# Kernel tuning notes

Measured on AMD Instinct MI355X. Metric: run time of the kernel, lower is better.

## Reference

```python
import jax, jax.numpy as jnp
import numpy as np

N_NODES = 100000
N_EDGES = 3200000
F_IN = 512
HIDDEN = 16
N_LABELS = 64


def _degree_norms(edge_src, edge_dst, n):
    # DGL GraphConv norm='both': src side uses out-degree, dst side uses in-degree,
    # both clamped to min 1, raised to -1/2.
    ones = jnp.ones(edge_src.shape[0], dtype=jnp.float32)
    deg_out = jax.ops.segment_sum(ones, edge_src, num_segments=n)
    deg_in = jax.ops.segment_sum(ones, edge_dst, num_segments=n)
    norm_src = jax.lax.rsqrt(jnp.maximum(deg_out, 1.0))
    norm_dst = jax.lax.rsqrt(jnp.maximum(deg_in, 1.0))
    return norm_src, norm_dst


def setup_inputs() -> dict:
    key = jax.random.key(0)
    k_x, k_s, k_d, k_w1, k_b1, k_w2, k_b2 = jax.random.split(key, 7)
    features = jax.random.normal(k_x, (N_NODES, F_IN), dtype=jnp.float32)
    edge_src = jax.random.randint(k_s, (N_EDGES,), 0, N_NODES, dtype=jnp.int64)
    edge_dst = jax.random.randint(k_d, (N_EDGES,), 0, N_NODES, dtype=jnp.int64)
    # GraphConv params (glorot-ish scale)
    W1 = jax.random.normal(k_w1, (F_IN, HIDDEN), dtype=jnp.float32) * (1.0 / np.sqrt(F_IN))
    b1 = jnp.zeros((HIDDEN,), dtype=jnp.float32)
    W2 = jax.random.normal(k_w2, (HIDDEN, N_LABELS), dtype=jnp.float32) * (1.0 / np.sqrt(HIDDEN))
    b2 = jnp.zeros((N_LABELS,), dtype=jnp.float32)
    return {"features": features, "W1": W1, "b1": b1, "W2": W2, "b2": b2,
            "edge_src": edge_src, "edge_dst": edge_dst}


def reference(features, W1, b1, W2, b2, edge_src, edge_dst):
    n = features.shape[0]
    norm_src, norm_dst = _degree_norms(edge_src, edge_dst, n)

    # Layer 1: in_feats (512) > out_feats (16) -> DGL projects first, then aggregates.
    h = features * norm_src[:, None]          # [N, 512]
    h = h @ W1                                 # [N, 16]
    h = jax.ops.segment_sum(h[edge_src], edge_dst, num_segments=n)  # SpMM gather+scatter
    h = h * norm_dst[:, None] + b1
    h = jax.nn.relu(h)  # GraphConv activation; outer F.relu is idempotent

    # Layer 2: in_feats (16) <= out_feats (64) -> DGL aggregates first, then projects.
    h2 = h * norm_src[:, None]                 # [N, 16]
    h2 = jax.ops.segment_sum(h2[edge_src], edge_dst, num_segments=n)
    h2 = h2 * norm_dst[:, None]
    out = h2 @ W2 + b2                          # [N, 64]
    return out
```

## Files before the change

kernel.cpp:

```cpp
#include <hip/hip_runtime.h>

#define N_NODES 100000
#define N_EDGES 3200000
#define F_IN 512
#define HIDDEN 16
#define N_LABELS 64

#define BW 128
#define NBUCK ((N_NODES + BW - 1) / BW)
#define NCB 256
#define SCAN_N (NBUCK * NCB)
#define SCAN_BLKS ((SCAN_N + 1023) / 1024)
#define CAP 10240

__global__ __launch_bounds__(256) void count_kernel(
        const int* __restrict__ es, const int* __restrict__ ed,
        int* __restrict__ Msrc, int* __restrict__ Mdst) {
    __shared__ int h1[NBUCK], h2[NBUCK];
    const int tid = threadIdx.x, g = blockIdx.x;
    for (int i = tid; i < NBUCK; i += 256) { h1[i] = 0; h2[i] = 0; }
    __syncthreads();
    for (int i = g * 256 + tid; i < N_EDGES; i += NCB * 256) {
        atomicAdd(&h1[es[i] >> 7], 1);
        atomicAdd(&h2[ed[i] >> 7], 1);
    }
    __syncthreads();
    for (int i = tid; i < NBUCK; i += 256) {
        Msrc[i * NCB + g] = h1[i];
        Mdst[i * NCB + g] = h2[i];
    }
}

__global__ __launch_bounds__(256) void scanA_kernel(int* __restrict__ a, int* __restrict__ bsum) {
    __shared__ int s[256];
    const int tid = threadIdx.x;
    const int base = blockIdx.x * 1024 + tid * 4;
    int4 v = make_int4(0, 0, 0, 0);
    if (base + 3 < SCAN_N) v = *(const int4*)(a + base);
    else {
        if (base + 0 < SCAN_N) v.x = a[base + 0];
        if (base + 1 < SCAN_N) v.y = a[base + 1];
        if (base + 2 < SCAN_N) v.z = a[base + 2];
        if (base + 3 < SCAN_N) v.w = a[base + 3];
    }
    const int lsum = v.x + v.y + v.z + v.w;
    s[tid] = lsum;
    __syncthreads();
    for (int off = 1; off < 256; off <<= 1) {
        int t = (tid >= off) ? s[tid - off] : 0;
        __syncthreads();
        s[tid] += t;
        __syncthreads();
    }
    int e0 = s[tid] - lsum;
    int e1 = e0 + v.x, e2 = e1 + v.y, e3 = e2 + v.z;
    if (base + 3 < SCAN_N) *(int4*)(a + base) = make_int4(e0, e1, e2, e3);
    else {
        if (base + 0 < SCAN_N) a[base + 0] = e0;
        if (base + 1 < SCAN_N) a[base + 1] = e1;
        if (base + 2 < SCAN_N) a[base + 2] = e2;
        if (base + 3 < SCAN_N) a[base + 3] = e3;
    }
    if (tid == 255) bsum[blockIdx.x] = s[255];
}

__global__ void scanB_kernel(int* __restrict__ bsum) {
    __shared__ int s[256];
    const int tid = threadIdx.x;
    int v = (tid < SCAN_BLKS) ? bsum[tid] : 0;
    s[tid] = v;
    __syncthreads();
    for (int off = 1; off < 256; off <<= 1) {
        int t = (tid >= off) ? s[tid - off] : 0;
        __syncthreads();
        s[tid] += t;
        __syncthreads();
    }
    if (tid < SCAN_BLKS) bsum[tid] = s[tid] - v;
}

__global__ __launch_bounds__(256) void scanC_kernel(int* __restrict__ a, const int* __restrict__ bsum) {
    const int base = blockIdx.x * 1024 + threadIdx.x * 4;
    const int b = bsum[blockIdx.x];
    if (base + 3 < SCAN_N) {
        int4 v = *(int4*)(a + base);
        v.x += b; v.y += b; v.z += b; v.w += b;
        *(int4*)(a + base) = v;
    } else {
        for (int j = 0; j < 4; ++j) if (base + j < SCAN_N) a[base + j] += b;
    }
}

__global__ __launch_bounds__(256) void scatter_kernel(
        const int* __restrict__ es, const int* __restrict__ ed,
        const int* __restrict__ Ssrc, const int* __restrict__ Sdst,
        unsigned* __restrict__ pairs, unsigned char* __restrict__ srcb) {
    __shared__ int c1[NBUCK], c2[NBUCK];
    const int tid = threadIdx.x, g = blockIdx.x;
    for (int i = tid; i < NBUCK; i += 256) {
        c1[i] = Ssrc[i * NCB + g];
        c2[i] = Sdst[i * NCB + g];
    }
    __syncthreads();
    for (int i = g * 256 + tid; i < N_EDGES; i += NCB * 256) {
        int s = es[i], d = ed[i];
        int p2 = atomicAdd(&c2[d >> 7], 1);
        pairs[p2] = ((unsigned)(d & 127) << 17) | (unsigned)s;
        int p1 = atomicAdd(&c1[s >> 7], 1);
        srcb[p1] = (unsigned char)(s & 127);
    }
}

__global__ __launch_bounds__(256) void csr_kernel(
        const int* __restrict__ Sdst, unsigned* __restrict__ pairs,
        int* __restrict__ row_ptr, float* __restrict__ norm_dst) {
    __shared__ unsigned buf[CAP];
    __shared__ int hist[BW], scn[BW], cur[BW];
    const int b = blockIdx.x, tid = threadIdx.x;
    const int base  = Sdst[b * NCB];
    const int nextb = (b == NBUCK - 1) ? N_EDGES : Sdst[(b + 1) * NCB];
    const int nb = nextb - base;
    const bool fits = (nb <= CAP);
    if (tid < BW) hist[tid] = 0;
    __syncthreads();
    for (int i = tid; i < nb; i += 256) {
        unsigned pk = pairs[base + i];
        if (fits) buf[i] = pk;
        atomicAdd(&hist[pk >> 17], 1);
    }
    __syncthreads();
    if (tid < BW) scn[tid] = hist[tid];
    __syncthreads();
    for (int off = 1; off < BW; off <<= 1) {
        int t = 0;
        if (tid < BW && tid >= off) t = scn[tid - off];
        __syncthreads();
        if (tid < BW) scn[tid] += t;
        __syncthreads();
    }
    if (tid < BW) {
        int e = scn[tid] - hist[tid];
        cur[tid] = e;
        int node = b * BW + tid;
        if (node <= N_NODES) row_ptr[node] = base + e;
        if (node < N_NODES) norm_dst[node] = rsqrtf(fmaxf((float)hist[tid], 1.0f));
    }
    __syncthreads();
    if (fits) {
        for (int i = tid; i < nb; i += 256) {
            unsigned pk = buf[i];
            int pos = atomicAdd(&cur[pk >> 17], 1);
            pairs[base + pos] = pk & 0x1FFFFu;
        }
    } else {
        for (int i = tid; i < nb; i += 256)
            pairs[base + i] &= 0x1FFFFu;
    }
}

__global__ __launch_bounds__(256) void srcdeg_kernel(
        const int* __restrict__ Ssrc, const unsigned char* __restrict__ srcb,
        float* __restrict__ norm_src) {
    __shared__ int hist[BW];
    const int b = blockIdx.x, tid = threadIdx.x;
    const int base  = Ssrc[b * NCB];
    const int nextb = (b == NBUCK - 1) ? N_EDGES : Ssrc[(b + 1) * NCB];
    const int nb = nextb - base;
    if (tid < BW) hist[tid] = 0;
    __syncthreads();
    for (int i = tid; i < nb; i += 256)
        atomicAdd(&hist[srcb[base + i]], 1);
    __syncthreads();
    if (tid < BW) {
        int node = b * BW + tid;
        if (node < N_NODES) norm_src[node] = rsqrtf(fmaxf((float)hist[tid], 1.0f));
    }
}

#define P1_ROWS 256
#define P1_CH 32
#define KSPLIT 2
#define KH (F_IN / KSPLIT)
#define P1_CHUNKS (KH / P1_CH)
#define P1_BLKS ((N_NODES + P1_ROWS - 1) / P1_ROWS)

#define GLD16(gp, lp) __builtin_amdgcn_global_load_lds( \
    (const __attribute__((address_space(1))) unsigned int*)(gp), \
    (__attribute__((address_space(3))) unsigned int*)(lp), 16, 0, 0)

__global__ __launch_bounds__(256, 2) void proj1_kernel(
        const float* __restrict__ X, const float* __restrict__ W1,
        float* __restrict__ P0, float* __restrict__ P1) {
    __shared__ float xs[2][P1_ROWS * P1_CH];
    __shared__ float w1c[KH * HIDDEN];

    const int tid = threadIdx.x;
    const int node0 = blockIdx.x * P1_ROWS;
    const int z = blockIdx.y;

    const int srow0 = tid >> 3;
    const int scg   = tid & 7;
    const int wbase = tid & 192;

    for (int i = tid; i < KH * HIDDEN / 4; i += 256)
        ((float4*)w1c)[i] = ((const float4*)(W1 + (size_t)z * KH * HIDDEN))[i];

    {
        const float* Xc = X + (size_t)z * KH;
#pragma unroll
        for (int it = 0; it < 8; ++it) {
            int row = srow0 + it * 32;
            int grow = node0 + row;
            if (grow > N_NODES - 1) grow = N_NODES - 1;
            int cg = scg ^ ((row >> 2) & 7);
            const float* gp = Xc + (size_t)grow * F_IN + cg * 4;
            float* lp = &xs[0][(size_t)(it * 256 + wbase) * 4];
            GLD16(gp, lp);
        }
    }
    __syncthreads();

    const int rg = tid >> 2;
    const int kq = (tid & 3) * 4;

    float acc[4][4];
#pragma unroll
    for (int a = 0; a < 4; ++a)
#pragma unroll
        for (int b = 0; b < 4; ++b) acc[a][b] = 0.f;

    for (int cc = 0; cc < P1_CHUNKS; ++cc) {
        const int cur = cc & 1;

        if (cc + 1 < P1_CHUNKS) {
            const float* Xc = X + (size_t)z * KH + (size_t)(cc + 1) * P1_CH;
#pragma unroll
            for (int it = 0; it < 8; ++it) {
                int row = srow0 + it * 32;
                int grow = node0 + row;
                if (grow > N_NODES - 1) grow = N_NODES - 1;
                int cg = scg ^ ((row >> 2) & 7);
                const float* gp = Xc + (size_t)grow * F_IN + cg * 4;
                float* lp = &xs[cur ^ 1][(size_t)(it * 256 + wbase) * 4];
                GLD16(gp, lp);
            }
        }

        const float* xb = &xs[cur][0];
#pragma unroll
        for (int kk4 = 0; kk4 < 8; ++kk4) {
            float4 w0 = *((const float4*)&w1c[(cc * P1_CH + kk4 * 4 + 0) * HIDDEN + kq]);
            float4 w1 = *((const float4*)&w1c[(cc * P1_CH + kk4 * 4 + 1) * HIDDEN + kq]);
            float4 w2 = *((const float4*)&w1c[(cc * P1_CH + kk4 * 4 + 2) * HIDDEN + kq]);
            float4 w3 = *((const float4*)&w1c[(cc * P1_CH + kk4 * 4 + 3) * HIDDEN + kq]);
#pragma unroll
            for (int a = 0; a < 4; ++a) {
                int row = rg * 4 + a;
                int sw  = (row >> 2) & 7;
                float4 xv = *((const float4*)&xb[row * P1_CH + ((kk4 ^ sw) * 4)]);
                acc[a][0] += xv.x * w0.x; acc[a][1] += xv.x * w0.y;
                acc[a][2] += xv.x * w0.z; acc[a][3] += xv.x * w0.w;
                acc[a][0] += xv.y * w1.x; acc[a][1] += xv.y * w1.y;
                acc[a][2] += xv.y * w1.z; acc[a][3] += xv.y * w1.w;
                acc[a][0] += xv.z * w2.x; acc[a][1] += xv.z * w2.y;
                acc[a][2] += xv.z * w2.z; acc[a][3] += xv.z * w2.w;
                acc[a][0] += xv.w * w3.x; acc[a][1] += xv.w * w3.y;
                acc[a][2] += xv.w * w3.z; acc[a][3] += xv.w * w3.w;
            }
        }

        __syncthreads();
    }

    float* Pz = z ? P1 : P0;
#pragma unroll
    for (int a = 0; a < 4; ++a) {
        int gn = node0 + rg * 4 + a;
        if (gn < N_NODES)
            *((float4*)(Pz + (size_t)gn * HIDDEN + kq)) =
                make_float4(acc[a][0], acc[a][1], acc[a][2], acc[a][3]);
    }
}

__global__ void reduce1_kernel(const float* __restrict__ P0, const float* __restrict__ P1,
                               const float* __restrict__ norm_src, float* __restrict__ H1) {
    int gid = blockIdx.x * blockDim.x + threadIdx.x;
    if (gid < N_NODES * 4) {
        float4 a = ((const float4*)P0)[gid];
        float4 b = ((const float4*)P1)[gid];
        float ns = norm_src[gid >> 2];
        ((float4*)H1)[gid] = make_float4((a.x + b.x) * ns, (a.y + b.y) * ns,
                                         (a.z + b.z) * ns, (a.w + b.w) * ns);
    }
}

__global__ __launch_bounds__(256) void spmm1_kernel(
        const int* __restrict__ rp, const int* __restrict__ col,
        const float* __restrict__ H1, const float* __restrict__ norm_dst,
        const float* __restrict__ norm_src, const float* __restrict__ b1,
        float* __restrict__ H1b) {
    int tid = threadIdx.x;
    int node = blockIdx.x * 16 + (tid >> 4);
    int k = tid & 15;
    if (node >= N_NODES) return;
    int beg = rp[node], end = rp[node + 1];
    float acc = 0.f;
    int j = beg;
    for (; j + 3 < end; j += 4) {
        int s0 = col[j], s1 = col[j + 1], s2 = col[j + 2], s3 = col[j + 3];
        float v0 = H1[(size_t)s0 * HIDDEN + k];
        float v1 = H1[(size_t)s1 * HIDDEN + k];
        float v2 = H1[(size_t)s2 * HIDDEN + k];
        float v3 = H1[(size_t)s3 * HIDDEN + k];
        acc += v0 + v1 + v2 + v3;
    }
    for (; j < end; ++j) acc += H1[(size_t)col[j] * HIDDEN + k];
    float v = fmaxf(acc * norm_dst[node] + b1[k], 0.f) * norm_src[node];
    H1b[(size_t)node * HIDDEN + k] = v;
}

__global__ __launch_bounds__(256) void spmm2_final_kernel(
        const int* __restrict__ rp, const int* __restrict__ col,
        const float* __restrict__ H1b, const float* __restrict__ norm_dst,
        const float* __restrict__ W2, const float* __restrict__ b2,
        float* __restrict__ out) {
    __shared__ float w2s[HIDDEN * N_LABELS];
    int tid = threadIdx.x;
    ((float4*)w2s)[tid] = ((const float4*)W2)[tid];
    __syncthreads();

    int node = blockIdx.x * 16 + (tid >> 4);
    int k = tid & 15;
    if (node >= N_NODES) return;
    int beg = rp[node], end = rp[node + 1];
    float acc = 0.f;
    int j = beg;
    for (; j + 3 < end; j += 4) {
        int s0 = col[j], s1 = col[j + 1], s2 = col[j + 2], s3 = col[j + 3];
        float v0 = H1b[(size_t)s0 * HIDDEN + k];
        float v1 = H1b[(size_t)s1 * HIDDEN + k];
        float v2 = H1b[(size_t)s2 * HIDDEN + k];
        float v3 = H1b[(size_t)s3 * HIDDEN + k];
        acc += v0 + v1 + v2 + v3;
    }
    for (; j < end; ++j) acc += H1b[(size_t)col[j] * HIDDEN + k];
    acc *= norm_dst[node];

    float4 o = ((const float4*)b2)[k];
#pragma unroll
    for (int jj = 0; jj < HIDDEN; ++jj) {
        float hj = __shfl(acc, jj, 16);
        float4 w = *((const float4*)&w2s[jj * N_LABELS + 4 * k]);
        o.x += hj * w.x; o.y += hj * w.y; o.z += hj * w.z; o.w += hj * w.w;
    }
    ((float4*)out)[(size_t)node * 16 + k] = o;
}

extern "C" void kernel_launch(void* const* d_in, const int* in_sizes, int n_in,
                              void* d_out, int out_size, void* d_ws, size_t ws_size,
                              hipStream_t stream) {
    const float* X  = (const float*)d_in[0];
    const float* W1 = (const float*)d_in[1];
    const float* b1 = (const float*)d_in[2];
    const float* W2 = (const float*)d_in[3];
    const float* b2 = (const float*)d_in[4];
    const int* es   = (const int*)d_in[5];
    const int* ed   = (const int*)d_in[6];
    float* out = (float*)d_out;

    char* ws = (char*)d_ws;
    float* norm_src = (float*)ws;  ws += (size_t)N_NODES * 4;
    float* norm_dst = (float*)ws;  ws += (size_t)N_NODES * 4;
    int*   row_ptr  = (int*)ws;    ws += 400016;
    char*  R1 = ws;                ws += (size_t)N_NODES * HIDDEN * 4;
    char*  R2 = ws;                ws += (size_t)N_NODES * HIDDEN * 4;
    char*  R3 = ws;

    unsigned char* srcb = (unsigned char*)R1;
    float* P0  = (float*)R1;
    float* H1  = (float*)R1;
    int*   Sdst = (int*)R2;
    int*   Ssrc = (int*)(R2 + 800768);
    int*   bs1  = (int*)(R2 + 1601536);
    int*   bs2  = (int*)(R2 + 1602560);
    float* P1   = (float*)R2;
    float* H1b  = (float*)R2;
    unsigned* pairs = (unsigned*)R3;
    int*   col  = (int*)R3;

    count_kernel<<<NCB, 256, 0, stream>>>(es, ed, Ssrc, Sdst);
    scanA_kernel<<<SCAN_BLKS, 256, 0, stream>>>(Sdst, bs1);
    scanA_kernel<<<SCAN_BLKS, 256, 0, stream>>>(Ssrc, bs2);
    scanB_kernel<<<1, 256, 0, stream>>>(bs1);
    scanB_kernel<<<1, 256, 0, stream>>>(bs2);
    scanC_kernel<<<SCAN_BLKS, 256, 0, stream>>>(Sdst, bs1);
    scanC_kernel<<<SCAN_BLKS, 256, 0, stream>>>(Ssrc, bs2);
    scatter_kernel<<<NCB, 256, 0, stream>>>(es, ed, Ssrc, Sdst, pairs, srcb);
    csr_kernel<<<NBUCK, 256, 0, stream>>>(Sdst, pairs, row_ptr, norm_dst);
    srcdeg_kernel<<<NBUCK, 256, 0, stream>>>(Ssrc, srcb, norm_src);
    proj1_kernel<<<dim3(P1_BLKS, KSPLIT), 256, 0, stream>>>(X, W1, P0, P1);
    reduce1_kernel<<<(N_NODES * 4 + 255) / 256, 256, 0, stream>>>(P0, P1, norm_src, H1);
    spmm1_kernel<<<(N_NODES + 15) / 16, 256, 0, stream>>>(row_ptr, col, H1, norm_dst, norm_src, b1, H1b);
    spmm2_final_kernel<<<(N_NODES + 15) / 16, 256, 0, stream>>>(row_ptr, col, H1b, norm_dst, W2, b2, out);
}
```

Before: 598.8 us.

## Replace full CSR build with padded bucket scatter and shared-memory atomic aggregation

```diff
diff --git a/kernel.cpp b/kernel.cpp
--- a/kernel.cpp
+++ b/kernel.cpp
@@ -7,173 +7,36 @@
 #define N_LABELS 64
 
 #define BW 128
-#define NBUCK ((N_NODES + BW - 1) / BW)
+#define NBUCK 782
 #define NCB 256
-#define SCAN_N (NBUCK * NCB)
-#define SCAN_BLKS ((SCAN_N + 1023) / 1024)
-#define CAP 10240
-
-__global__ __launch_bounds__(256) void count_kernel(
+#define EPC (N_EDGES / NCB)
+#define PADB 4544
+
+__global__ __launch_bounds__(512) void scatter2_kernel(
         const int* __restrict__ es, const int* __restrict__ ed,
-        int* __restrict__ Msrc, int* __restrict__ Mdst) {
-    __shared__ int h1[NBUCK], h2[NBUCK];
+        int* __restrict__ gcur, int* __restrict__ deg,
+        unsigned* __restrict__ pairs) {
+    __shared__ int hist[NBUCK];
+    __shared__ int curL[NBUCK];
     const int tid = threadIdx.x, g = blockIdx.x;
-    for (int i = tid; i < NBUCK; i += 256) { h1[i] = 0; h2[i] = 0; }
-    __syncthreads();
-    for (int i = g * 256 + tid; i < N_EDGES; i += NCB * 256) {
-        atomicAdd(&h1[es[i] >> 7], 1);
-        atomicAdd(&h2[ed[i] >> 7], 1);
-    }
-    __syncthreads();
-    for (int i = tid; i < NBUCK; i += 256) {
-        Msrc[i * NCB + g] = h1[i];
-        Mdst[i * NCB + g] = h2[i];
-    }
-}
-
-__global__ __launch_bounds__(256) void scanA_kernel(int* __restrict__ a, int* __restrict__ bsum) {
-    __shared__ int s[256];
-    const int tid = threadIdx.x;
-    const int base = blockIdx.x * 1024 + tid * 4;
-    int4 v = make_int4(0, 0, 0, 0);
-    if (base + 3 < SCAN_N) v = *(const int4*)(a + base);
-    else {
-        if (base + 0 < SCAN_N) v.x = a[base + 0];
-        if (base + 1 < SCAN_N) v.y = a[base + 1];
-        if (base + 2 < SCAN_N) v.z = a[base + 2];
-        if (base + 3 < SCAN_N) v.w = a[base + 3];
-    }
-    const int lsum = v.x + v.y + v.z + v.w;
-    s[tid] = lsum;
-    __syncthreads();
-    for (int off = 1; off < 256; off <<= 1) {
-        int t = (tid >= off) ? s[tid - off] : 0;
-        __syncthreads();
-        s[tid] += t;
-        __syncthreads();
-    }
-    int e0 = s[tid] - lsum;
-    int e1 = e0 + v.x, e2 = e1 + v.y, e3 = e2 + v.z;
-    if (base + 3 < SCAN_N) *(int4*)(a + base) = make_int4(e0, e1, e2, e3);
-    else {
-        if (base + 0 < SCAN_N) a[base + 0] = e0;
-        if (base + 1 < SCAN_N) a[base + 1] = e1;
-        if (base + 2 < SCAN_N) a[base + 2] = e2;
-        if (base + 3 < SCAN_N) a[base + 3] = e3;
-    }
-    if (tid == 255) bsum[blockIdx.x] = s[255];
-}
-
-__global__ void scanB_kernel(int* __restrict__ bsum) {
-    __shared__ int s[256];
-    const int tid = threadIdx.x;
-    int v = (tid < SCAN_BLKS) ? bsum[tid] : 0;
-    s[tid] = v;
-    __syncthreads();
-    for (int off = 1; off < 256; off <<= 1) {
-        int t = (tid >= off) ? s[tid - off] : 0;
-        __syncthreads();
-        s[tid] += t;
-        __syncthreads();
-    }
-    if (tid < SCAN_BLKS) bsum[tid] = s[tid] - v;
-}
-
-__global__ __launch_bounds__(256) void scanC_kernel(int* __restrict__ a, const int* __restrict__ bsum) {
-    const int base = blockIdx.x * 1024 + threadIdx.x * 4;
-    const int b = bsum[blockIdx.x];
-    if (base + 3 < SCAN_N) {
-        int4 v = *(int4*)(a + base);
-        v.x += b; v.y += b; v.z += b; v.w += b;
-        *(int4*)(a + base) = v;
-    } else {
-        for (int j = 0; j < 4; ++j) if (base + j < SCAN_N) a[base + j] += b;
-    }
-}
-
-__global__ __launch_bounds__(256) void scatter_kernel(
-        const int* __restrict__ es, const int* __restrict__ ed,
-        const int* __restrict__ Ssrc, const int* __restrict__ Sdst,
-        unsigned* __restrict__ pairs, unsigned char* __restrict__ srcb) {
-    __shared__ int c1[NBUCK], c2[NBUCK];
-    const int tid = threadIdx.x, g = blockIdx.x;
-    for (int i = tid; i < NBUCK; i += 256) {
-        c1[i] = Ssrc[i * NCB + g];
-        c2[i] = Sdst[i * NCB + g];
-    }
-    __syncthreads();
-    for (int i = g * 256 + tid; i < N_EDGES; i += NCB * 256) {
-        int s = es[i], d = ed[i];
-        int p2 = atomicAdd(&c2[d >> 7], 1);
-        pairs[p2] = ((unsigned)(d & 127) << 17) | (unsigned)s;
-        int p1 = atomicAdd(&c1[s >> 7], 1);
-        srcb[p1] = (unsigned char)(s & 127);
-    }
-}
-
-__global__ __launch_bounds__(256) void csr_kernel(
-        const int* __restrict__ Sdst, unsigned* __restrict__ pairs,
-        int* __restrict__ row_ptr, float* __restrict__ norm_dst) {
-    __shared__ unsigned buf[CAP];
-    __shared__ int hist[BW], scn[BW], cur[BW];
-    const int b = blockIdx.x, tid = threadIdx.x;
-    const int base  = Sdst[b * NCB];
-    const int nextb = (b == NBUCK - 1) ? N_EDGES : Sdst[(b + 1) * NCB];
-    const int nb = nextb - base;
-    const bool fits = (nb <= CAP);
-    if (tid < BW) hist[tid] = 0;
-    __syncthreads();
-    for (int i = tid; i < nb; i += 256) {
-        unsigned pk = pairs[base + i];
-        if (fits) buf[i] = pk;
-        atomicAdd(&hist[pk >> 17], 1);
-    }
-    __syncthreads();
-    if (tid < BW) scn[tid] = hist[tid];
-    __syncthreads();
-    for (int off = 1; off < BW; off <<= 1) {
-        int t = 0;
-        if (tid < BW && tid >= off) t = scn[tid - off];
-        __syncthreads();
-        if (tid < BW) scn[tid] += t;
-        __syncthreads();
-    }
-    if (tid < BW) {
-        int e = scn[tid] - hist[tid];
-        cur[tid] = e;
-        int node = b * BW + tid;
-        if (node <= N_NODES) row_ptr[node] = base + e;
-        if (node < N_NODES) norm_dst[node] = rsqrtf(fmaxf((float)hist[tid], 1.0f));
-    }
-    __syncthreads();
-    if (fits) {
-        for (int i = tid; i < nb; i += 256) {
-            unsigned pk = buf[i];
-            int pos = atomicAdd(&cur[pk >> 17], 1);
-            pairs[base + pos] = pk & 0x1FFFFu;
-        }
-    } else {
-        for (int i = tid; i < nb; i += 256)
-            pairs[base + i] &= 0x1FFFFu;
-    }
-}
-
-__global__ __launch_bounds__(256) void srcdeg_kernel(
-        const int* __restrict__ Ssrc, const unsigned char* __restrict__ srcb,
-        float* __restrict__ norm_src) {
-    __shared__ int hist[BW];
-    const int b = blockIdx.x, tid = threadIdx.x;
-    const int base  = Ssrc[b * NCB];
-    const int nextb = (b == NBUCK - 1) ? N_EDGES : Ssrc[(b + 1) * NCB];
-    const int nb = nextb - base;
-    if (tid < BW) hist[tid] = 0;
-    __syncthreads();
-    for (int i = tid; i < nb; i += 256)
-        atomicAdd(&hist[srcb[base + i]], 1);
-    __syncthreads();
-    if (tid < BW) {
-        int node = b * BW + tid;
-        if (node < N_NODES) norm_src[node] = rsqrtf(fmaxf((float)hist[tid], 1.0f));
+    const int e0 = g * EPC;
+    for (int i = tid; i < NBUCK; i += 512) hist[i] = 0;
+    __syncthreads();
+    for (int i = tid; i < EPC; i += 512)
+        atomicAdd(&hist[ed[e0 + i] >> 7], 1);
+    __syncthreads();
+    for (int i = tid; i < NBUCK; i += 512) {
+        int h = hist[i];
+        int old = h ? atomicAdd(&gcur[i], h) : 0;
+        curL[i] = i * PADB + old;
+    }
+    __syncthreads();
+    for (int i = tid; i < EPC; i += 512) {
+        int d = ed[e0 + i], s = es[e0 + i];
+        atomicAdd(&deg[s], 1);
+        int p = atomicAdd(&curL[d >> 7], 1);
+        if (p < (d >> 7) * PADB + PADB)
+            pairs[p] = ((unsigned)(d & 127) << 17) | (unsigned)s;
     }
 }
 
@@ -283,77 +146,96 @@
 }
 
 __global__ void reduce1_kernel(const float* __restrict__ P0, const float* __restrict__ P1,
-                               const float* __restrict__ norm_src, float* __restrict__ H1) {
+                               const int* __restrict__ deg, float* __restrict__ H1) {
     int gid = blockIdx.x * blockDim.x + threadIdx.x;
     if (gid < N_NODES * 4) {
         float4 a = ((const float4*)P0)[gid];
         float4 b = ((const float4*)P1)[gid];
-        float ns = norm_src[gid >> 2];
+        float ns = rsqrtf(fmaxf((float)deg[gid >> 2], 1.f));
         ((float4*)H1)[gid] = make_float4((a.x + b.x) * ns, (a.y + b.y) * ns,
                                          (a.z + b.z) * ns, (a.w + b.w) * ns);
     }
 }
 
-__global__ __launch_bounds__(256) void spmm1_kernel(
-        const int* __restrict__ rp, const int* __restrict__ col,
-        const float* __restrict__ H1, const float* __restrict__ norm_dst,
-        const float* __restrict__ norm_src, const float* __restrict__ b1,
-        float* __restrict__ H1b) {
-    int tid = threadIdx.x;
-    int node = blockIdx.x * 16 + (tid >> 4);
-    int k = tid & 15;
-    if (node >= N_NODES) return;
-    int beg = rp[node], end = rp[node + 1];
-    float acc = 0.f;
-    int j = beg;
-    for (; j + 3 < end; j += 4) {
-        int s0 = col[j], s1 = col[j + 1], s2 = col[j + 2], s3 = col[j + 3];
-        float v0 = H1[(size_t)s0 * HIDDEN + k];
-        float v1 = H1[(size_t)s1 * HIDDEN + k];
-        float v2 = H1[(size_t)s2 * HIDDEN + k];
-        float v3 = H1[(size_t)s3 * HIDDEN + k];
-        acc += v0 + v1 + v2 + v3;
-    }
-    for (; j < end; ++j) acc += H1[(size_t)col[j] * HIDDEN + k];
-    float v = fmaxf(acc * norm_dst[node] + b1[k], 0.f) * norm_src[node];
-    H1b[(size_t)node * HIDDEN + k] = v;
-}
-
-__global__ __launch_bounds__(256) void spmm2_final_kernel(
-        const int* __restrict__ rp, const int* __restrict__ col,
-        const float* __restrict__ H1b, const float* __restrict__ norm_dst,
-        const float* __restrict__ W2, const float* __restrict__ b2,
-        float* __restrict__ out) {
+__global__ __launch_bounds__(512) void agg1_kernel(
+        const int* __restrict__ gcur, const unsigned* __restrict__ pairs,
+        const float* __restrict__ H1, const int* __restrict__ deg,
+        const float* __restrict__ b1, float* __restrict__ H1b) {
+    __shared__ float acc[BW][HIDDEN + 1];
+    __shared__ int histd[BW];
+    const int b = blockIdx.x, tid = threadIdx.x;
+    for (int i = tid; i < BW * (HIDDEN + 1); i += 512) (&acc[0][0])[i] = 0.f;
+    if (tid < BW) histd[tid] = 0;
+    __syncthreads();
+    const int cnt = min(gcur[b], PADB);
+    const int base = b * PADB;
+    const int pi = tid >> 4, k = tid & 15;
+#pragma unroll 4
+    for (int i = pi; i < cnt; i += 32) {
+        unsigned pk = pairs[base + i];
+        int d = pk >> 17, s = pk & 0x1FFFF;
+        float v = H1[(size_t)s * HIDDEN + k];
+        atomicAdd(&acc[d][k], v);
+        if (k == 0) atomicAdd(&histd[d], 1);
+    }
+    __syncthreads();
+    for (int d = pi; d < BW; d += 32) {
+        int node = b * BW + d;
+        if (node < N_NODES) {
+            float nd = rsqrtf(fmaxf((float)histd[d], 1.f));
+            float ns = rsqrtf(fmaxf((float)deg[node], 1.f));
+            H1b[(size_t)node * HIDDEN + k] =
+                fmaxf(acc[d][k] * nd + b1[k], 0.f) * ns;
+        }
+    }
+}
+
+__global__ __launch_bounds__(512) void agg2_kernel(
+        const int* __restrict__ gcur, const unsigned* __restrict__ pairs,
+        const float* __restrict__ H1b, const float* __restrict__ W2,
+        const float* __restrict__ b2, float* __restrict__ out) {
+    __shared__ float acc[BW][HIDDEN + 1];
+    __shared__ int histd[BW];
     __shared__ float w2s[HIDDEN * N_LABELS];
-    int tid = threadIdx.x;
-    ((float4*)w2s)[tid] = ((const float4*)W2)[tid];
-    __syncthreads();
-
-    int node = blockIdx.x * 16 + (tid >> 4);
-    int k = tid & 15;
-    if (node >= N_NODES) return;
-    int beg = rp[node], end = rp[node + 1];
-    float acc = 0.f;
-    int j = beg;
-    for (; j + 3 < end; j += 4) {
-        int s0 = col[j], s1 = col[j + 1], s2 = col[j + 2], s3 = col[j + 3];
-        float v0 = H1b[(size_t)s0 * HIDDEN + k];
-        float v1 = H1b[(size_t)s1 * HIDDEN + k];
-        float v2 = H1b[(size_t)s2 * HIDDEN + k];
-        float v3 = H1b[(size_t)s3 * HIDDEN + k];
-        acc += v0 + v1 + v2 + v3;
-    }
-    for (; j < end; ++j) acc += H1b[(size_t)col[j] * HIDDEN + k];
-    acc *= norm_dst[node];
-
-    float4 o = ((const float4*)b2)[k];
-#pragma unroll
-    for (int jj = 0; jj < HIDDEN; ++jj) {
-        float hj = __shfl(acc, jj, 16);
-        float4 w = *((const float4*)&w2s[jj * N_LABELS + 4 * k]);
-        o.x += hj * w.x; o.y += hj * w.y; o.z += hj * w.z; o.w += hj * w.w;
-    }
-    ((float4*)out)[(size_t)node * 16 + k] = o;
+    const int b = blockIdx.x, tid = threadIdx.x;
+    for (int i = tid; i < BW * (HIDDEN + 1); i += 512) (&acc[0][0])[i] = 0.f;
+    if (tid < BW) histd[tid] = 0;
+    if (tid < HIDDEN * N_LABELS / 4) ((float4*)w2s)[tid] = ((const float4*)W2)[tid];
+    __syncthreads();
+    const int cnt = min(gcur[b], PADB);
+    const int base = b * PADB;
+    const int pi = tid >> 4, k = tid & 15;
+#pragma unroll 4
+    for (int i = pi; i < cnt; i += 32) {
+        unsigned pk = pairs[base + i];
+        int d = pk >> 17, s = pk & 0x1FFFF;
+        float v = H1b[(size_t)s * HIDDEN + k];
+        atomicAdd(&acc[d][k], v);
+        if (k == 0) atomicAdd(&histd[d], 1);
+    }
+    __syncthreads();
+    {
+        const int d = tid >> 2, cq = tid & 3;
+        int node = b * BW + d;
+        if (node < N_NODES) {
+            float nd = rsqrtf(fmaxf((float)histd[d], 1.f));
+            float h[HIDDEN];
+#pragma unroll
+            for (int j = 0; j < HIDDEN; ++j) h[j] = acc[d][j] * nd;
+#pragma unroll
+            for (int c4 = 0; c4 < 4; ++c4) {
+                int c = cq * 16 + c4 * 4;
+                float4 o = *((const float4*)(b2 + c));
+#pragma unroll
+                for (int j = 0; j < HIDDEN; ++j) {
+                    float4 w = *((const float4*)&w2s[j * N_LABELS + c]);
+                    o.x += h[j] * w.x; o.y += h[j] * w.y;
+                    o.z += h[j] * w.z; o.w += h[j] * w.w;
+                }
+                *((float4*)(out + (size_t)node * N_LABELS + c)) = o;
+            }
+        }
+    }
 }
 
 extern "C" void kernel_launch(void* const* d_in, const int* in_sizes, int n_in,
@@ -369,37 +251,18 @@
     float* out = (float*)d_out;
 
     char* ws = (char*)d_ws;
-    float* norm_src = (float*)ws;  ws += (size_t)N_NODES * 4;
-    float* norm_dst = (float*)ws;  ws += (size_t)N_NODES * 4;
-    int*   row_ptr  = (int*)ws;    ws += 400016;
-    char*  R1 = ws;                ws += (size_t)N_NODES * HIDDEN * 4;
-    char*  R2 = ws;                ws += (size_t)N_NODES * HIDDEN * 4;
-    char*  R3 = ws;
-
-    unsigned char* srcb = (unsigned char*)R1;
-    float* P0  = (float*)R1;
-    float* H1  = (float*)R1;
-    int*   Sdst = (int*)R2;
-    int*   Ssrc = (int*)(R2 + 800768);
-    int*   bs1  = (int*)(R2 + 1601536);
-    int*   bs2  = (int*)(R2 + 1602560);
-    float* P1   = (float*)R2;
-    float* H1b  = (float*)R2;
-    unsigned* pairs = (unsigned*)R3;
-    int*   col  = (int*)R3;
-
-    count_kernel<<<NCB, 256, 0, stream>>>(es, ed, Ssrc, Sdst);
-    scanA_kernel<<<SCAN_BLKS, 256, 0, stream>>>(Sdst, bs1);
-    scanA_kernel<<<SCAN_BLKS, 256, 0, stream>>>(Ssrc, bs2);
-    scanB_kernel<<<1, 256, 0, stream>>>(bs1);
-    scanB_kernel<<<1, 256, 0, stream>>>(bs2);
-    scanC_kernel<<<SCAN_BLKS, 256, 0, stream>>>(Sdst, bs1);
-    scanC_kernel<<<SCAN_BLKS, 256, 0, stream>>>(Ssrc, bs2);
-    scatter_kernel<<<NCB, 256, 0, stream>>>(es, ed, Ssrc, Sdst, pairs, srcb);
-    csr_kernel<<<NBUCK, 256, 0, stream>>>(Sdst, pairs, row_ptr, norm_dst);
-    srcdeg_kernel<<<NBUCK, 256, 0, stream>>>(Ssrc, srcb, norm_src);
+    int*   deg  = (int*)ws;      ws += 400000;
+    int*   gcur = (int*)ws;      ws += 3136;
+    float* P0   = (float*)ws;    ws += (size_t)N_NODES * HIDDEN * 4;
+    float* P1   = (float*)ws;    ws += (size_t)N_NODES * HIDDEN * 4;
+    unsigned* pairs = (unsigned*)ws;
+    float* H1  = P0;
+    float* H1b = P1;
+
+    hipMemsetAsync(deg, 0, 403136, stream);
+    scatter2_kernel<<<NCB, 512, 0, stream>>>(es, ed, gcur, deg, pairs);
     proj1_kernel<<<dim3(P1_BLKS, KSPLIT), 256, 0, stream>>>(X, W1, P0, P1);
-    reduce1_kernel<<<(N_NODES * 4 + 255) / 256, 256, 0, stream>>>(P0, P1, norm_src, H1);
-    spmm1_kernel<<<(N_NODES + 15) / 16, 256, 0, stream>>>(row_ptr, col, H1, norm_dst, norm_src, b1, H1b);
-    spmm2_final_kernel<<<(N_NODES + 15) / 16, 256, 0, stream>>>(row_ptr, col, H1b, norm_dst, W2, b2, out);
-}
+    reduce1_kernel<<<(N_NODES * 4 + 255) / 256, 256, 0, stream>>>(P0, P1, deg, H1);
+    agg1_kernel<<<NBUCK, 512, 0, stream>>>(gcur, pairs, H1, deg, b1, H1b);
+    agg2_kernel<<<NBUCK, 512, 0, stream>>>(gcur, pairs, H1b, W2, b2, out);
+}
```

New measurement: 1.194 ms. +99.3%, slower.
